# Optimization experiments

Hardware: AMD Instinct MI355X
Metric: run time of the kernel (lower is better)

Reference implementation:

```python
import jax, jax.numpy as jnp
import numpy as np

NHRZ, BATCH, NU, NY, NH = 2048, 128, 64, 64, 256  # NH even; half-size rotation params


def setup_inputs() -> dict:
    key = jax.random.key(0)
    ks = jax.random.split(key, 9)
    H = NH // 2
    damping = 0.9  # dampingConstantInitial < 1.0
    return {
        "y0": jax.random.normal(ks[0], (BATCH, NY), jnp.float32),
        "U": jax.random.normal(ks[1], (NHRZ, BATCH, NU), jnp.float32),
        # torch init: lmbd_cont_real = -log(damping) * ones(H); imag ~ U[0,1)
        "lmbd_cont_real": jnp.full((H,), -np.log(damping), jnp.float32),
        "lmbd_cont_imag": jax.random.uniform(ks[2], (H,), jnp.float32),
        "B": jax.random.normal(ks[3], (NH, NU), jnp.float32) / np.sqrt(NU),
        "Wy2x": jax.random.normal(ks[4], (NH, NY), jnp.float32) / np.sqrt(NY),
        "by2x": jax.random.normal(ks[5], (NH,), jnp.float32) * 0.01,
        "Wx2y": jax.random.normal(ks[6], (NY, NH), jnp.float32) / np.sqrt(NH),
        "bx2y": jax.random.normal(ks[7], (NY,), jnp.float32) * 0.01,
    }


def reference(y0, U, lmbd_cont_real, lmbd_cont_imag, B, Wy2x, by2x, Wx2y, bx2y):
    H = lmbd_cont_real.shape[0]  # Nhidden // 2
    r = jnp.exp(-jnp.abs(lmbd_cont_real))
    theta = (np.pi / 2) * lmbd_cont_imag
    lr = r * jnp.cos(theta)   # [H]
    li = r * jnp.sin(theta)   # [H]
    nf = jnp.sqrt(1.0 - jnp.exp(-2.0 * jnp.abs(lmbd_cont_real)))
    nf2 = jnp.concatenate((nf, nf))                       # [2H]
    Bu = jnp.einsum('tbu,hu->tbh', U, B) * nf2            # [T, B, 2H]
    x0 = y0 @ Wy2x.T + by2x                               # [B, 2H]

    # A = [[diag(lr), -diag(li)], [diag(li), diag(lr)]]; x_new = x @ A.T = A x
    def step(x, bu):
        x1, x2 = x[..., :H], x[..., H:]
        xn = jnp.concatenate((lr * x1 - li * x2, li * x1 + lr * x2), axis=-1) + bu
        return xn, xn

    _, Xs = jax.lax.scan(step, x0, Bu)                    # [T, B, 2H]
    X = jnp.concatenate((x0[None], Xs), axis=0)           # [T+1, B, 2H]
    Y = X @ Wx2y.T + bx2y                                 # [T+1, B, Ny]
    return Y
```

## Files before the change

kernel.cpp:

```cpp
#include <hip/hip_runtime.h>
#include <hip/hip_bf16.h>

typedef __bf16 bf16x8 __attribute__((ext_vector_type(8)));
typedef __bf16 bf16x4 __attribute__((ext_vector_type(4)));
typedef float  f32x4  __attribute__((ext_vector_type(4)));

constexpr int kNHRZ = 2048, kBATCH = 128, kNU = 64, kNY = 64, kNH = 256, kH = 128;
constexpr int kCHUNK = 256, kNCHUNK = kNHRZ / kCHUNK;
constexpr int kTS = 16, kBT = 2, kM = kTS * kBT;
constexpr int kNSUB = kCHUNK / kTS;

constexpr int U_STR  = 72;
constexpr int BT_STR = 36;
constexpr int X_STR  = 264;

constexpr int OFF_U  = 0;
constexpr int OFF_BU = OFF_U + 2 * kM * U_STR * 2;
constexpr int OFF_X  = OFF_BU + kNH * BT_STR * 2;
constexpr int SMEM1  = OFF_X;
constexpr int SMEM2  = OFF_X + kM * X_STR * 2;

__device__ inline bf16x8 pack8(float4 a, float4 b) {
    bf16x8 v;
    v[0] = (__bf16)a.x; v[1] = (__bf16)a.y; v[2] = (__bf16)a.z; v[3] = (__bf16)a.w;
    v[4] = (__bf16)b.x; v[5] = (__bf16)b.y; v[6] = (__bf16)b.z; v[7] = (__bf16)b.w;
    return v;
}

template <bool FINAL>
__global__ __launch_bounds__(256, 2) void scan_mfma(
    const float* __restrict__ U,
    const float* __restrict__ lre,
    const float* __restrict__ lim,
    const float* __restrict__ Bmat,
    const float* __restrict__ Wx2y,
    const float* __restrict__ bx2y,
    const float* __restrict__ starts,
    float* __restrict__ ends,
    float* __restrict__ out)
{
    extern __shared__ char smem[];
    __bf16* Us  = (__bf16*)(smem + OFF_U);
    __bf16* BuT = (__bf16*)(smem + OFF_BU);
    __bf16* Xs  = (__bf16*)(smem + OFF_X);

    const int tid  = threadIdx.x;
    const int lane = tid & 63;
    const int w    = tid >> 6;
    const int lw   = lane & 15;
    const int lg   = lane >> 4;
    const int blk  = blockIdx.x;
    const int c    = blk >> 6;
    const int bp   = blk & 63;
    const int bglob = bp * 2;
    const int t0   = c * kCHUNK;

    bf16x8 Bf[2][4];
#pragma unroll
    for (int nt = 0; nt < 4; ++nt) {
        const int hre = w * 32 + (nt & 1) * 16 + lw;
        const int h   = hre + (nt >> 1) * kH;
        const float ab = fabsf(lre[hre]);
        const float nf = sqrtf(fmaxf(0.0f, 1.0f - expf(-2.0f * ab)));
#pragma unroll
        for (int ks = 0; ks < 2; ++ks) {
            const float* p = Bmat + h * kNU + ks * 32 + lg * 8;
            float4 f0 = ((const float4*)p)[0];
            float4 f1 = ((const float4*)p)[1];
            f0.x *= nf; f0.y *= nf; f0.z *= nf; f0.w *= nf;
            f1.x *= nf; f1.y *= nf; f1.z *= nf; f1.w *= nf;
            Bf[ks][nt] = pack8(f0, f1);
        }
    }

    bf16x8 Wf[8][2];
    float  bias[2] = {0.f, 0.f};
    if constexpr (FINAL) {
#pragma unroll
        for (int nt = 0; nt < 2; ++nt) {
            const int y = (w >> 1) * 32 + nt * 16 + lw;
            bias[nt] = bx2y[y];
#pragma unroll
            for (int ks = 0; ks < 8; ++ks) {
                const float* p = Wx2y + y * kNH + ks * 32 + lg * 8;
                Wf[ks][nt] = pack8(((const float4*)p)[0], ((const float4*)p)[1]);
            }
        }
    }

    const int hm = w * 32 + (lane & 31);
    const int bl = lane >> 5;
    float lr, li;
    {
        const float ab = fabsf(lre[hm]);
        const float r  = expf(-ab);
        const float th = 1.5707963267948966f * lim[hm];
        lr = r * cosf(th);
        li = r * sinf(th);
    }
    float x1, x2;
    if constexpr (FINAL) {
        const size_t sb = ((size_t)c * kBATCH + bglob + bl) * kNH;
        x1 = starts[sb + hm];
        x2 = starts[sb + hm + kH];
    } else {
        x1 = 0.0f; x2 = 0.0f;
    }

    const int sm = tid >> 3, sq = tid & 7;
    const int st_t = sm & 15, st_b = sm >> 4;
    const float* uptr0 =
        U + ((size_t)(t0 + st_t) * kBATCH + (bglob + st_b)) * kNU + sq * 8;

    float4 u0 = ((const float4*)uptr0)[0];
    float4 u1 = ((const float4*)uptr0)[1];

#pragma unroll 1
    for (int s = 0; s < kNSUB; ++s) {
        __bf16* Uc = Us + (s & 1) * (kM * U_STR);

        *(bf16x8*)&Uc[sm * U_STR + sq * 8] = pack8(u0, u1);
        __syncthreads();

        if constexpr (!FINAL) {
            if (s + 1 < kNSUB) {
                const float* p = uptr0 + (size_t)(s + 1) * kTS * kBATCH * kNU;
                u0 = ((const float4*)p)[0];
                u1 = ((const float4*)p)[1];
            }
        }

        {
            f32x4 acc[2][4] = {};
#pragma unroll
            for (int ks = 0; ks < 2; ++ks) {
                bf16x8 a0 = *(const bf16x8*)&Uc[(lw)      * U_STR + ks * 32 + lg * 8];
                bf16x8 a1 = *(const bf16x8*)&Uc[(16 + lw) * U_STR + ks * 32 + lg * 8];
#pragma unroll
                for (int nt = 0; nt < 4; ++nt) {
                    acc[0][nt] = __builtin_amdgcn_mfma_f32_16x16x32_bf16(a0, Bf[ks][nt], acc[0][nt], 0, 0, 0);
                    acc[1][nt] = __builtin_amdgcn_mfma_f32_16x16x32_bf16(a1, Bf[ks][nt], acc[1][nt], 0, 0, 0);
                }
            }
#pragma unroll
            for (int mt = 0; mt < 2; ++mt)
#pragma unroll
                for (int nt = 0; nt < 4; ++nt) {
                    const int h = w * 32 + (nt & 1) * 16 + lw + (nt >> 1) * kH;
                    bf16x4 v;
                    v[0] = (__bf16)acc[mt][nt][0]; v[1] = (__bf16)acc[mt][nt][1];
                    v[2] = (__bf16)acc[mt][nt][2]; v[3] = (__bf16)acc[mt][nt][3];
                    *(bf16x4*)&BuT[h * BT_STR + mt * 16 + lg * 4] = v;
                }
        }

        {
            bf16x4 qr[4], qi[4];
#pragma unroll
            for (int k = 0; k < 4; ++k) {
                qr[k] = *(const bf16x4*)&BuT[hm * BT_STR + bl * 16 + k * 4];
                qi[k] = *(const bf16x4*)&BuT[(hm + kH) * BT_STR + bl * 16 + k * 4];
            }
#pragma unroll
            for (int t = 0; t < kTS; ++t) {
                const float bu1 = (float)qr[t >> 2][t & 3];
                const float bu2 = (float)qi[t >> 2][t & 3];
                const float n1 = fmaf(lr, x1, fmaf(-li, x2, bu1));
                const float n2 = fmaf(li, x1, fmaf(lr, x2, bu2));
                x1 = n1; x2 = n2;
                if constexpr (FINAL) {
                    const int m = bl * 16 + t;
                    Xs[m * X_STR + hm]      = (__bf16)x1;
                    Xs[m * X_STR + kH + hm] = (__bf16)x2;
                }
            }
        }

        if constexpr (FINAL) {
            __syncthreads();
            if (s + 1 < kNSUB) {
                const float* p = uptr0 + (size_t)(s + 1) * kTS * kBATCH * kNU;
                u0 = ((const float4*)p)[0];
                u1 = ((const float4*)p)[1];
            }
            f32x4 acc2[2] = {};
            const int mtY = w & 1;
#pragma unroll
            for (int ks = 0; ks < 8; ++ks) {
                bf16x8 a = *(const bf16x8*)&Xs[(mtY * 16 + lw) * X_STR + ks * 32 + lg * 8];
                acc2[0] = __builtin_amdgcn_mfma_f32_16x16x32_bf16(a, Wf[ks][0], acc2[0], 0, 0, 0);
                acc2[1] = __builtin_amdgcn_mfma_f32_16x16x32_bf16(a, Wf[ks][1], acc2[1], 0, 0, 0);
            }
#pragma unroll
            for (int i = 0; i < 4; ++i) {
                const int t = t0 + s * kTS + lg * 4 + i;
                float* orow = out + ((size_t)(1 + t) * kBATCH + bglob + mtY) * kNY +
                              (w >> 1) * 32 + lw;
#pragma unroll
                for (int nt = 0; nt < 2; ++nt)
                    orow[nt * 16] = acc2[nt][i] + bias[nt];
            }
        }
    }

    if constexpr (!FINAL) {
        const size_t eb = ((size_t)c * kBATCH + bglob + bl) * kNH;
        ends[eb + hm]      = x1;
        ends[eb + hm + kH] = x2;
    }
}

__global__ __launch_bounds__(128) void combine_kernel(
    const float* __restrict__ y0, const float* __restrict__ Wy2x,
    const float* __restrict__ by2x, const float* __restrict__ lre,
    const float* __restrict__ lim, const float* __restrict__ ends,
    float* __restrict__ starts)
{
    const int b  = blockIdx.x;
    const int hm = threadIdx.x;

    const float ab = fabsf(lre[hm]);
    const float r  = expf(-ab);
    const float th = 1.5707963267948966f * lim[hm];
    float lr = r * cosf(th);
    float li = r * sinf(th);
    float pr = lr, pi = li;
#pragma unroll
    for (int k = 0; k < 8; ++k) {
        const float nr = pr * pr - pi * pi;
        const float ni = 2.0f * pr * pi;
        pr = nr; pi = ni;
    }

    float s1 = by2x[hm];
    float s2 = by2x[hm + kH];
#pragma unroll 8
    for (int q = 0; q < kNY; ++q) {
        const float yv = y0[b * kNY + q];
        s1 = fmaf(Wy2x[hm * kNY + q], yv, s1);
        s2 = fmaf(Wy2x[(hm + kH) * kNY + q], yv, s2);
    }

    for (int c = 0; c < kNCHUNK; ++c) {
        const size_t base = ((size_t)c * kBATCH + b) * kNH;
        starts[base + hm]      = s1;
        starts[base + hm + kH] = s2;
        const float e1 = ends[base + hm];
        const float e2 = ends[base + hm + kH];
        const float n1 = fmaf(pr, s1, fmaf(-pi, s2, e1));
        const float n2 = fmaf(pi, s1, fmaf(pr, s2, e2));
        s1 = n1; s2 = n2;
    }
}

__global__ __launch_bounds__(64) void y0_kernel(
    const float* __restrict__ starts, const float* __restrict__ Wx2y,
    const float* __restrict__ bx2y, float* __restrict__ out)
{
    const int b = blockIdx.x;
    const int y = threadIdx.x;
    const float* x0 = starts + (size_t)b * kNH;
    float acc = bx2y[y];
#pragma unroll 4
    for (int h = 0; h < kNH; h += 4) {
        float4 xv = *(const float4*)&x0[h];
        float4 wv = *(const float4*)&Wx2y[y * kNH + h];
        acc = fmaf(wv.x, xv.x, acc);
        acc = fmaf(wv.y, xv.y, acc);
        acc = fmaf(wv.z, xv.z, acc);
        acc = fmaf(wv.w, xv.w, acc);
    }
    out[(size_t)b * kNY + y] = acc;
}

extern "C" void kernel_launch(void* const* d_in, const int* in_sizes, int n_in,
                              void* d_out, int out_size, void* d_ws, size_t ws_size,
                              hipStream_t stream) {
    const float* y0   = (const float*)d_in[0];
    const float* U    = (const float*)d_in[1];
    const float* lre  = (const float*)d_in[2];
    const float* lim  = (const float*)d_in[3];
    const float* Bmat = (const float*)d_in[4];
    const float* Wy2x = (const float*)d_in[5];
    const float* by2x = (const float*)d_in[6];
    const float* Wx2y = (const float*)d_in[7];
    const float* bx2y = (const float*)d_in[8];
    float* out = (float*)d_out;

    float* ends   = (float*)d_ws;
    float* starts = ends + (size_t)kNCHUNK * kBATCH * kNH;

    const int grid = kNCHUNK * (kBATCH / kBT);

    scan_mfma<false><<<grid, 256, SMEM1, stream>>>(
        U, lre, lim, Bmat, nullptr, nullptr, nullptr, ends, nullptr);
    combine_kernel<<<kBATCH, 128, 0, stream>>>(
        y0, Wy2x, by2x, lre, lim, ends, starts);
    y0_kernel<<<kBATCH, 64, 0, stream>>>(starts, Wx2y, bx2y, out);
    scan_mfma<true><<<grid, 256, SMEM2, stream>>>(
        U, lre, lim, Bmat, Wx2y, bx2y, starts, nullptr, out);
}
```

Before: 77.09 us.

## Split scan into local pass with output and linear correction pass

The first chunked-scan pass now computes outputs from a zero-start local scan and writes Y directly. The second pass no longer reloads U or recomputes Bu. It only propagates the homogeneous decay of each chunk's carry-in state and adds its projection through Wx2y to the output already written. This removes a full re-read of U and the input GEMM from the second pass. In exchange the output is written twice and read-modify-written once, and the first pass becomes heavier.

```diff
diff --git a/kernel.cpp b/kernel.cpp
--- a/kernel.cpp
+++ b/kernel.cpp
@@ -17,8 +17,8 @@
 constexpr int OFF_U  = 0;
 constexpr int OFF_BU = OFF_U + 2 * kM * U_STR * 2;
 constexpr int OFF_X  = OFF_BU + kNH * BT_STR * 2;
-constexpr int SMEM1  = OFF_X;
-constexpr int SMEM2  = OFF_X + kM * X_STR * 2;
+constexpr int SMEM1  = OFF_X + kM * X_STR * 2;
+constexpr int SMEM2  = 2 * kM * X_STR * 2;
 
 __device__ inline bf16x8 pack8(float4 a, float4 b) {
     bf16x8 v;
@@ -27,15 +27,13 @@
     return v;
 }
 
-template <bool FINAL>
-__global__ __launch_bounds__(256, 2) void scan_mfma(
+__global__ __launch_bounds__(256, 2) void scan_local(
     const float* __restrict__ U,
     const float* __restrict__ lre,
     const float* __restrict__ lim,
     const float* __restrict__ Bmat,
     const float* __restrict__ Wx2y,
     const float* __restrict__ bx2y,
-    const float* __restrict__ starts,
     float* __restrict__ ends,
     float* __restrict__ out)
 {
@@ -74,17 +72,15 @@
     }
 
     bf16x8 Wf[8][2];
-    float  bias[2] = {0.f, 0.f};
-    if constexpr (FINAL) {
-#pragma unroll
-        for (int nt = 0; nt < 2; ++nt) {
-            const int y = (w >> 1) * 32 + nt * 16 + lw;
-            bias[nt] = bx2y[y];
-#pragma unroll
-            for (int ks = 0; ks < 8; ++ks) {
-                const float* p = Wx2y + y * kNH + ks * 32 + lg * 8;
-                Wf[ks][nt] = pack8(((const float4*)p)[0], ((const float4*)p)[1]);
-            }
+    float  bias[2];
+#pragma unroll
+    for (int nt = 0; nt < 2; ++nt) {
+        const int y = (w >> 1) * 32 + nt * 16 + lw;
+        bias[nt] = bx2y[y];
+#pragma unroll
+        for (int ks = 0; ks < 8; ++ks) {
+            const float* p = Wx2y + y * kNH + ks * 32 + lg * 8;
+            Wf[ks][nt] = pack8(((const float4*)p)[0], ((const float4*)p)[1]);
         }
     }
 
@@ -98,14 +94,7 @@
         lr = r * cosf(th);
         li = r * sinf(th);
     }
-    float x1, x2;
-    if constexpr (FINAL) {
-        const size_t sb = ((size_t)c * kBATCH + bglob + bl) * kNH;
-        x1 = starts[sb + hm];
-        x2 = starts[sb + hm + kH];
-    } else {
-        x1 = 0.0f; x2 = 0.0f;
-    }
+    float x1 = 0.0f, x2 = 0.0f;
 
     const int sm = tid >> 3, sq = tid & 7;
     const int st_t = sm & 15, st_b = sm >> 4;
@@ -121,14 +110,6 @@
 
         *(bf16x8*)&Uc[sm * U_STR + sq * 8] = pack8(u0, u1);
         __syncthreads();
-
-        if constexpr (!FINAL) {
-            if (s + 1 < kNSUB) {
-                const float* p = uptr0 + (size_t)(s + 1) * kTS * kBATCH * kNU;
-                u0 = ((const float4*)p)[0];
-                u1 = ((const float4*)p)[1];
-            }
-        }
 
         {
             f32x4 acc[2][4] = {};
@@ -168,45 +149,126 @@
                 const float n1 = fmaf(lr, x1, fmaf(-li, x2, bu1));
                 const float n2 = fmaf(li, x1, fmaf(lr, x2, bu2));
                 x1 = n1; x2 = n2;
-                if constexpr (FINAL) {
-                    const int m = bl * 16 + t;
-                    Xs[m * X_STR + hm]      = (__bf16)x1;
-                    Xs[m * X_STR + kH + hm] = (__bf16)x2;
-                }
+                const int m = bl * 16 + t;
+                Xs[m * X_STR + hm]      = (__bf16)x1;
+                Xs[m * X_STR + kH + hm] = (__bf16)x2;
             }
         }
 
-        if constexpr (FINAL) {
-            __syncthreads();
-            if (s + 1 < kNSUB) {
-                const float* p = uptr0 + (size_t)(s + 1) * kTS * kBATCH * kNU;
-                u0 = ((const float4*)p)[0];
-                u1 = ((const float4*)p)[1];
-            }
-            f32x4 acc2[2] = {};
-            const int mtY = w & 1;
-#pragma unroll
-            for (int ks = 0; ks < 8; ++ks) {
-                bf16x8 a = *(const bf16x8*)&Xs[(mtY * 16 + lw) * X_STR + ks * 32 + lg * 8];
-                acc2[0] = __builtin_amdgcn_mfma_f32_16x16x32_bf16(a, Wf[ks][0], acc2[0], 0, 0, 0);
-                acc2[1] = __builtin_amdgcn_mfma_f32_16x16x32_bf16(a, Wf[ks][1], acc2[1], 0, 0, 0);
-            }
-#pragma unroll
-            for (int i = 0; i < 4; ++i) {
-                const int t = t0 + s * kTS + lg * 4 + i;
-                float* orow = out + ((size_t)(1 + t) * kBATCH + bglob + mtY) * kNY +
-                              (w >> 1) * 32 + lw;
-#pragma unroll
-                for (int nt = 0; nt < 2; ++nt)
-                    orow[nt * 16] = acc2[nt][i] + bias[nt];
-            }
-        }
-    }
-
-    if constexpr (!FINAL) {
+        __syncthreads();
+        if (s + 1 < kNSUB) {
+            const float* p = uptr0 + (size_t)(s + 1) * kTS * kBATCH * kNU;
+            u0 = ((const float4*)p)[0];
+            u1 = ((const float4*)p)[1];
+        }
+        f32x4 acc2[2] = {};
+        const int mtY = w & 1;
+#pragma unroll
+        for (int ks = 0; ks < 8; ++ks) {
+            bf16x8 a = *(const bf16x8*)&Xs[(mtY * 16 + lw) * X_STR + ks * 32 + lg * 8];
+            acc2[0] = __builtin_amdgcn_mfma_f32_16x16x32_bf16(a, Wf[ks][0], acc2[0], 0, 0, 0);
+            acc2[1] = __builtin_amdgcn_mfma_f32_16x16x32_bf16(a, Wf[ks][1], acc2[1], 0, 0, 0);
+        }
+#pragma unroll
+        for (int i = 0; i < 4; ++i) {
+            const int t = t0 + s * kTS + lg * 4 + i;
+            float* orow = out + ((size_t)(1 + t) * kBATCH + bglob + mtY) * kNY +
+                          (w >> 1) * 32 + lw;
+#pragma unroll
+            for (int nt = 0; nt < 2; ++nt)
+                orow[nt * 16] = acc2[nt][i] + bias[nt];
+        }
+    }
+
+    {
         const size_t eb = ((size_t)c * kBATCH + bglob + bl) * kNH;
         ends[eb + hm]      = x1;
         ends[eb + hm + kH] = x2;
+    }
+}
+
+__global__ __launch_bounds__(256, 2) void scan_corr(
+    const float* __restrict__ lre,
+    const float* __restrict__ lim,
+    const float* __restrict__ Wx2y,
+    const float* __restrict__ starts,
+    float* __restrict__ out)
+{
+    extern __shared__ char smem[];
+    __bf16* Xs = (__bf16*)smem;
+
+    const int tid  = threadIdx.x;
+    const int lane = tid & 63;
+    const int w    = tid >> 6;
+    const int lw   = lane & 15;
+    const int lg   = lane >> 4;
+    const int blk  = blockIdx.x;
+    const int c    = blk >> 6;
+    const int bp   = blk & 63;
+    const int bglob = bp * 2;
+    const int t0   = c * kCHUNK;
+
+    bf16x8 Wf[8][2];
+#pragma unroll
+    for (int nt = 0; nt < 2; ++nt) {
+        const int y = (w >> 1) * 32 + nt * 16 + lw;
+#pragma unroll
+        for (int ks = 0; ks < 8; ++ks) {
+            const float* p = Wx2y + y * kNH + ks * 32 + lg * 8;
+            Wf[ks][nt] = pack8(((const float4*)p)[0], ((const float4*)p)[1]);
+        }
+    }
+
+    const int hm = w * 32 + (lane & 31);
+    const int bl = lane >> 5;
+    float lr, li;
+    {
+        const float ab = fabsf(lre[hm]);
+        const float r  = expf(-ab);
+        const float th = 1.5707963267948966f * lim[hm];
+        lr = r * cosf(th);
+        li = r * sinf(th);
+    }
+    float c1, c2;
+    {
+        const size_t sb = ((size_t)c * kBATCH + bglob + bl) * kNH;
+        c1 = starts[sb + hm];
+        c2 = starts[sb + hm + kH];
+    }
+
+#pragma unroll 1
+    for (int s = 0; s < kNSUB; ++s) {
+        __bf16* Xc = Xs + (s & 1) * (kM * X_STR);
+
+#pragma unroll
+        for (int t = 0; t < kTS; ++t) {
+            const float n1 = fmaf(lr, c1, -li * c2);
+            const float n2 = fmaf(li, c1,  lr * c2);
+            c1 = n1; c2 = n2;
+            const int m = bl * 16 + t;
+            Xc[m * X_STR + hm]      = (__bf16)c1;
+            Xc[m * X_STR + kH + hm] = (__bf16)c2;
+        }
+
+        __syncthreads();
+
+        f32x4 acc2[2] = {};
+        const int mtY = w & 1;
+#pragma unroll
+        for (int ks = 0; ks < 8; ++ks) {
+            bf16x8 a = *(const bf16x8*)&Xc[(mtY * 16 + lw) * X_STR + ks * 32 + lg * 8];
+            acc2[0] = __builtin_amdgcn_mfma_f32_16x16x32_bf16(a, Wf[ks][0], acc2[0], 0, 0, 0);
+            acc2[1] = __builtin_amdgcn_mfma_f32_16x16x32_bf16(a, Wf[ks][1], acc2[1], 0, 0, 0);
+        }
+#pragma unroll
+        for (int i = 0; i < 4; ++i) {
+            const int t = t0 + s * kTS + lg * 4 + i;
+            float* orow = out + ((size_t)(1 + t) * kBATCH + bglob + mtY) * kNY +
+                          (w >> 1) * 32 + lw;
+#pragma unroll
+            for (int nt = 0; nt < 2; ++nt)
+                orow[nt * 16] += acc2[nt][i];
+        }
     }
 }
 
@@ -292,11 +354,11 @@
 
     const int grid = kNCHUNK * (kBATCH / kBT);
 
-    scan_mfma<false><<<grid, 256, SMEM1, stream>>>(
-        U, lre, lim, Bmat, nullptr, nullptr, nullptr, ends, nullptr);
+    scan_local<<<grid, 256, SMEM1, stream>>>(
+        U, lre, lim, Bmat, Wx2y, bx2y, ends, out);
     combine_kernel<<<kBATCH, 128, 0, stream>>>(
         y0, Wy2x, by2x, lre, lim, ends, starts);
     y0_kernel<<<kBATCH, 64, 0, stream>>>(starts, Wx2y, bx2y, out);
-    scan_mfma<true><<<grid, 256, SMEM2, stream>>>(
-        U, lre, lim, Bmat, Wx2y, bx2y, starts, nullptr, out);
-}
+    scan_corr<<<grid, 256, SMEM2, stream>>>(
+        lre, lim, Wx2y, starts, out);
+}
```

New measurement: 89.79 us. 1.16x slower.
